# Kernel optimization log

Hardware: AMD Instinct MI355X
Metric: run time of the kernel (lower is better)

The kernel has to match this reference:

```python
import jax, jax.numpy as jnp
import numpy as np

B, N_TOK, DIM, HEADS, FRAMES = 16, 1569, 768, 12, 8
HEAD_DIM = DIM // HEADS
N_SPACE = (N_TOK - 1) // FRAMES  # 196
EPS = 1e-6


def _ln(x, w, b):
    m = jnp.mean(x, axis=-1, keepdims=True)
    v = jnp.var(x, axis=-1, keepdims=True)
    return (x - m) * jax.lax.rsqrt(v + EPS) * w + b


def _sdpa(q, k, v):
    # q: [..., Sq, d], k/v: [..., Sk, d]
    s = jnp.einsum('...qd,...kd->...qk', q, k) * (HEAD_DIM ** -0.5)
    return jnp.einsum('...qk,...kd->...qd', jax.nn.softmax(s, axis=-1), v)


def _divided_attn(x, w_qkv, b_qkv, w_proj, b_proj, mode):
    # Faithful translation of DividedAttention.forward
    Bb, N, D = x.shape
    h, d, f = HEADS, HEAD_DIM, FRAMES
    n = (N - 1) // f
    qkv = x @ w_qkv + b_qkv                      # [B, N, 3D]
    q, k, v = jnp.split(qkv, 3, axis=-1)
    q, k, v = (t.reshape(Bb, N, h, d).transpose(0, 2, 1, 3) for t in (q, k, v))  # [B,h,N,d]
    # global cls-token attention over ALL tokens
    cls_out = _sdpa(q[:, :, :1], k, v)           # [B,h,1,d]
    # local tokens: split (f n) per einops pattern 'b (f n) d'
    q_, k_, v_ = (t[:, :, 1:].reshape(Bb, h, f, n, d) for t in (q, k, v))
    if mode == 'time':
        # '(b n) f d': batch over spatial positions, attend over frames
        q_, k_, v_ = (t.transpose(0, 1, 3, 2, 4) for t in (q_, k_, v_))  # [B,h,n,f,d]
        r = n
    else:
        # '(b f) n d': batch over frames, attend over spatial positions
        r = f
    cls_k = jnp.broadcast_to(k[:, :, None, :1], (Bb, h, r, 1, d))
    cls_v = jnp.broadcast_to(v[:, :, None, :1], (Bb, h, r, 1, d))
    out = _sdpa(q_,
                jnp.concatenate([cls_k, k_], axis=3),
                jnp.concatenate([cls_v, v_], axis=3))   # [B,h,r,seq,d]
    if mode == 'time':
        out = out.transpose(0, 1, 3, 2, 4)       # back to [B,h,f,n,d]
    out = out.reshape(Bb, h, N - 1, d)
    out = jnp.concatenate([cls_out, out], axis=2)          # [B,h,N,d]
    out = out.transpose(0, 2, 1, 3).reshape(Bb, N, D)      # 'b n (h d)'
    return out @ w_proj + b_proj


def setup_inputs() -> dict:
    key = jax.random.key(0)
    ks = jax.random.split(key, 8)
    s = 0.02
    return {
        'x': jax.random.normal(ks[0], (B, N_TOK, DIM), jnp.float32),
        'norm1_w': jnp.ones((DIM,), jnp.float32),
        'norm1_b': jnp.zeros((DIM,), jnp.float32),
        'norm2_w': jnp.ones((DIM,), jnp.float32),
        'norm2_b': jnp.zeros((DIM,), jnp.float32),
        'norm3_w': jnp.ones((DIM,), jnp.float32),
        'norm3_b': jnp.zeros((DIM,), jnp.float32),
        'time_qkv_w': jax.random.normal(ks[1], (DIM, 3 * DIM), jnp.float32) * s,
        'time_qkv_b': jnp.zeros((3 * DIM,), jnp.float32),
        'time_proj_w': jax.random.normal(ks[2], (DIM, DIM), jnp.float32) * s,
        'time_proj_b': jnp.zeros((DIM,), jnp.float32),
        'space_qkv_w': jax.random.normal(ks[3], (DIM, 3 * DIM), jnp.float32) * s,
        'space_qkv_b': jnp.zeros((3 * DIM,), jnp.float32),
        'space_proj_w': jax.random.normal(ks[4], (DIM, DIM), jnp.float32) * s,
        'space_proj_b': jnp.zeros((DIM,), jnp.float32),
        'mlp_w1': jax.random.normal(ks[5], (DIM, 4 * DIM), jnp.float32) * s,
        'mlp_b1': jnp.zeros((4 * DIM,), jnp.float32),
        'mlp_w2': jax.random.normal(ks[6], (4 * DIM, DIM), jnp.float32) * s,
        'mlp_b2': jnp.zeros((DIM,), jnp.float32),
    }


def reference(x, norm1_w, norm1_b, norm2_w, norm2_b, norm3_w, norm3_b,
              time_qkv_w, time_qkv_b, time_proj_w, time_proj_b,
              space_qkv_w, space_qkv_b, space_proj_w, space_proj_b,
              mlp_w1, mlp_b1, mlp_w2, mlp_b2):
    # DividedSpaceTimeBlock.forward
    t = _divided_attn(_ln(x, norm3_w, norm3_b),
                      time_qkv_w, time_qkv_b, time_proj_w, time_proj_b, 'time')
    x = x + t
    s = _divided_attn(_ln(x, norm1_w, norm1_b),
                      space_qkv_w, space_qkv_b, space_proj_w, space_proj_b, 'space')
    x = x + s
    h = jax.nn.gelu(_ln(x, norm2_w, norm2_b) @ mlp_w1 + mlp_b1)
    return x + h @ mlp_w2 + mlp_b2
```

## Files before the change

### kernel.cpp

```cpp
#include <hip/hip_runtime.h>
#include <cstdint>
#include <cstddef>

typedef unsigned short u16;
typedef __attribute__((ext_vector_type(8))) short short8;
typedef __attribute__((ext_vector_type(4))) float f32x4;

#define BB 16
#define NT 1569
#define DIM 768
#define NH 12
#define HD 64
#define FR 8
#define NS 196
#define MROWS (BB*NT)
#define NKEY 197

__device__ __forceinline__ float bf2f(u16 h) {
    return __uint_as_float(((unsigned int)h) << 16);
}
__device__ __forceinline__ u16 f2bf(float f) {
    unsigned int u = __float_as_uint(f);
    u += 0x7fff + ((u >> 16) & 1);
    return (u16)(u >> 16);
}
__device__ __forceinline__ void gload_lds16(const u16* g, u16* l) {
    __builtin_amdgcn_global_load_lds(
        (const __attribute__((address_space(1))) void*)g,
        (__attribute__((address_space(3))) void*)l, 16, 0, 0);
}

template<bool IBF>
__global__ __launch_bounds__(256) void ln_kernel(const void* __restrict__ xin,
        const float* __restrict__ w, const float* __restrict__ b,
        u16* __restrict__ out) {
    int row = blockIdx.x;
    size_t base = (size_t)row * DIM;
    int tid = threadIdx.x;
    float v0, v1, v2;
    if (IBF) {
        const u16* x = (const u16*)xin;
        v0 = bf2f(x[base + tid]); v1 = bf2f(x[base + tid + 256]); v2 = bf2f(x[base + tid + 512]);
    } else {
        const float* x = (const float*)xin;
        v0 = x[base + tid]; v1 = x[base + tid + 256]; v2 = x[base + tid + 512];
    }
    float s = v0 + v1 + v2;
    float q = v0*v0 + v1*v1 + v2*v2;
    #pragma unroll
    for (int o = 32; o >= 1; o >>= 1) {
        s += __shfl_xor(s, o, 64);
        q += __shfl_xor(q, o, 64);
    }
    __shared__ float rs[4], rq[4];
    int wave = tid >> 6, lane = tid & 63;
    if (lane == 0) { rs[wave] = s; rq[wave] = q; }
    __syncthreads();
    float S = rs[0]+rs[1]+rs[2]+rs[3];
    float Q = rq[0]+rq[1]+rq[2]+rq[3];
    float mean = S * (1.0f/DIM);
    float var  = Q * (1.0f/DIM) - mean*mean;
    float inv  = rsqrtf(var + 1e-6f);
    out[base+tid]     = f2bf((v0-mean)*inv*w[tid]     + b[tid]);
    out[base+tid+256] = f2bf((v1-mean)*inv*w[tid+256] + b[tid+256]);
    out[base+tid+512] = f2bf((v2-mean)*inv*w[tid+512] + b[tid+512]);
}

__global__ __launch_bounds__(256) void wconv_kernel(const float* __restrict__ in,
        u16* __restrict__ out, int K, int N) {
    __shared__ float tile[32][33];
    int n0 = blockIdx.x * 32, k0 = blockIdx.y * 32;
    int tx = threadIdx.x & 31, ty = threadIdx.x >> 5;
    #pragma unroll
    for (int i = 0; i < 32; i += 8)
        tile[ty+i][tx] = in[(size_t)(k0+ty+i)*N + n0+tx];
    __syncthreads();
    #pragma unroll
    for (int i = 0; i < 32; i += 8)
        out[(size_t)(n0+ty+i)*K + k0+tx] = f2bf(tile[tx][ty+i]);
}

template<int EPI, bool OBF, bool RBF>
__global__ __launch_bounds__(256) void gemm_kernel(
        const u16* __restrict__ A, const u16* __restrict__ BT,
        const float* __restrict__ bias, const void* __restrict__ resid,
        void* __restrict__ Cout, int M, int N, int K, int num_m, int num_n) {
    __shared__ u16 lsA[128*32];
    __shared__ u16 lsB[128*32];
    const int GRP = 16;
    int pid = blockIdx.x;
    int gsz = GRP * num_n;
    int gid = pid / gsz;
    int rem = pid - gid*gsz;
    int m0b = gid * GRP;
    int msz = num_m - m0b; if (msz > GRP) msz = GRP;
    int pm = m0b + rem % msz;
    int pn = rem / msz;
    int row0 = pm * 128, col0 = pn * 128;
    int tid = threadIdx.x;
    int wave = tid >> 6, lane = tid & 63;
    int wm = (wave >> 1) * 64, wn = (wave & 1) * 64;
    int lrow = lane & 15, quad = lane >> 4;
    int srow = lane >> 2, scol = (lane & 3) * 8;
    const u16* gAp[2]; const u16* gBp[2];
    u16* lA[2]; u16* lB[2];
    #pragma unroll
    for (int i = 0; i < 2; ++i) {
        int r = wave*32 + i*16 + srow;
        int gr = row0 + r; if (gr > M-1) gr = M-1;
        gAp[i] = A  + (size_t)gr*K + scol;
        gBp[i] = BT + (size_t)(col0 + r)*K + scol;
        lA[i] = &lsA[(wave*32 + i*16)*32];
        lB[i] = &lsB[(wave*32 + i*16)*32];
    }
    f32x4 acc[4][4] = {};
    for (int k0 = 0; k0 < K; k0 += 32) {
        #pragma unroll
        for (int i = 0; i < 2; ++i) {
            gload_lds16(gAp[i] + k0, lA[i]);
            gload_lds16(gBp[i] + k0, lB[i]);
        }
        __syncthreads();
        short8 af[4], bfr[4];
        #pragma unroll
        for (int t = 0; t < 4; ++t)
            af[t] = *(const short8*)&lsA[(wm + t*16 + lrow)*32 + quad*8];
        #pragma unroll
        for (int t = 0; t < 4; ++t)
            bfr[t] = *(const short8*)&lsB[(wn + t*16 + lrow)*32 + quad*8];
        #pragma unroll
        for (int i = 0; i < 4; ++i)
            #pragma unroll
            for (int j = 0; j < 4; ++j)
                acc[i][j] = __builtin_amdgcn_mfma_f32_16x16x32_bf16(af[i], bfr[j], acc[i][j], 0, 0, 0);
        __syncthreads();
    }
    #pragma unroll
    for (int i = 0; i < 4; ++i) {
      #pragma unroll
      for (int j = 0; j < 4; ++j) {
        int gn = col0 + wn + j*16 + lrow;
        float bv = bias[gn];
        #pragma unroll
        for (int r = 0; r < 4; ++r) {
            int gm = row0 + wm + i*16 + quad*4 + r;
            if (gm < M) {
                float v = acc[i][j][r] + bv;
                if (EPI == 1) {
                    size_t ridx = (size_t)gm*N + gn;
                    v += RBF ? bf2f(((const u16*)resid)[ridx]) : ((const float*)resid)[ridx];
                }
                if (EPI == 2) {
                    float z = 0.7978845608028654f*(v + 0.044715f*v*v*v);
                    float t = 1.0f - 2.0f/(__expf(2.0f*z) + 1.0f);
                    v = 0.5f*v*(1.0f + t);
                }
                if (OBF) ((u16*)Cout)[(size_t)gm*N + gn] = f2bf(v);
                else     ((float*)Cout)[(size_t)gm*N + gn] = v;
            }
        }
      }
    }
}

__global__ __launch_bounds__(256) void attn_cls_kernel(const u16* __restrict__ qkv,
        u16* __restrict__ out) {
    __shared__ float s[NT];
    __shared__ float qf[64];
    __shared__ float part[4][64];
    __shared__ float red[4];
    int b = blockIdx.x / NH, h = blockIdx.x % NH;
    size_t base = ((size_t)b*NT)*(3*DIM) + h*HD;
    int tid = threadIdx.x;
    if (tid < 64) qf[tid] = bf2f(qkv[base + tid]);
    __syncthreads();
    float lmax = -1e30f;
    for (int t = tid; t < NT; t += 256) {
        const u16* kp = qkv + base + (size_t)t*(3*DIM) + DIM;
        float a0=0,a1=0,a2=0,a3=0;
        #pragma unroll
        for (int d = 0; d < 64; d += 4) {
            a0 += qf[d]  *bf2f(kp[d]);
            a1 += qf[d+1]*bf2f(kp[d+1]);
            a2 += qf[d+2]*bf2f(kp[d+2]);
            a3 += qf[d+3]*bf2f(kp[d+3]);
        }
        float sc = (a0+a1+a2+a3)*0.125f;
        s[t] = sc;
        lmax = fmaxf(lmax, sc);
    }
    #pragma unroll
    for (int o = 32; o >= 1; o >>= 1) lmax = fmaxf(lmax, __shfl_xor(lmax, o, 64));
    if ((tid&63) == 0) red[tid>>6] = lmax;
    __syncthreads();
    float m = fmaxf(fmaxf(red[0],red[1]), fmaxf(red[2],red[3]));
    float lsum = 0.f;
    for (int t = tid; t < NT; t += 256) { float e = __expf(s[t]-m); s[t] = e; lsum += e; }
    #pragma unroll
    for (int o = 32; o >= 1; o >>= 1) lsum += __shfl_xor(lsum, o, 64);
    __syncthreads();
    if ((tid&63) == 0) red[tid>>6] = lsum;
    __syncthreads();
    float inv = 1.0f/(red[0]+red[1]+red[2]+red[3]);
    int d = tid & 63, g = tid >> 6;
    float a = 0.f;
    for (int t = g; t < NT; t += 4)
        a += s[t]*bf2f(qkv[base + (size_t)t*(3*DIM) + 2*DIM + d]);
    part[g][d] = a;
    __syncthreads();
    if (tid < 64) {
        float o = (part[0][tid]+part[1][tid]+part[2][tid]+part[3][tid])*inv;
        out[((size_t)b*NT)*DIM + h*HD + tid] = f2bf(o);
    }
}

__global__ __launch_bounds__(256) void attn_time_kernel(const u16* __restrict__ qkv,
        u16* __restrict__ out) {
    __shared__ float qs[8][68], ks[9][68], vs[9][68];
    __shared__ float pr[8][12];
    int bid = blockIdx.x;
    int n = bid % NS; int rem = bid / NS; int h = rem % NH; int b = rem / NH;
    size_t base = ((size_t)b*NT)*(3*DIM) + h*HD;
    int tid = threadIdx.x;
    for (int idx = tid; idx < 512; idx += 256) {
        int f = idx >> 6, d = idx & 63;
        int tok = 1 + f*NS + n;
        size_t p = base + (size_t)tok*(3*DIM) + d;
        qs[f][d]   = bf2f(qkv[p]);
        ks[f+1][d] = bf2f(qkv[p + DIM]);
        vs[f+1][d] = bf2f(qkv[p + 2*DIM]);
    }
    if (tid < 64) {
        ks[0][tid] = bf2f(qkv[base + DIM + tid]);
        vs[0][tid] = bf2f(qkv[base + 2*DIM + tid]);
    }
    __syncthreads();
    if (tid < 72) {
        int fq = tid / 9, kk = tid % 9;
        float a0=0,a1=0,a2=0,a3=0;
        #pragma unroll
        for (int d = 0; d < 64; d += 4) {
            a0 += qs[fq][d]  *ks[kk][d];
            a1 += qs[fq][d+1]*ks[kk][d+1];
            a2 += qs[fq][d+2]*ks[kk][d+2];
            a3 += qs[fq][d+3]*ks[kk][d+3];
        }
        pr[fq][kk] = (a0+a1+a2+a3)*0.125f;
    }
    __syncthreads();
    if (tid < 8) {
        float m = -1e30f;
        #pragma unroll
        for (int kk = 0; kk < 9; ++kk) m = fmaxf(m, pr[tid][kk]);
        float sum = 0.f;
        #pragma unroll
        for (int kk = 0; kk < 9; ++kk) { float e = __expf(pr[tid][kk]-m); pr[tid][kk] = e; sum += e; }
        float inv = 1.0f/sum;
        #pragma unroll
        for (int kk = 0; kk < 9; ++kk) pr[tid][kk] *= inv;
    }
    __syncthreads();
    for (int idx = tid; idx < 512; idx += 256) {
        int fq = idx >> 6, d = idx & 63;
        float a = 0.f;
        #pragma unroll
        for (int kk = 0; kk < 9; ++kk) a += pr[fq][kk]*vs[kk][d];
        int tok = 1 + fq*NS + n;
        out[((size_t)b*NT + tok)*DIM + h*HD + d] = f2bf(a);
    }
}

#define VSTR 232
__global__ __launch_bounds__(256, 2) void attn_space_kernel(const u16* __restrict__ qkv,
        u16* __restrict__ out) {
    __shared__ u16 VT[64*VSTR];
    __shared__ u16 Ps[4][16*VSTR];
    int bid = blockIdx.x;
    int b = bid / (NH*FR); int rem = bid % (NH*FR); int h = rem / FR; int f = rem % FR;
    size_t base = ((size_t)b*NT)*(3*DIM) + (size_t)h*HD;
    int tid = threadIdx.x;
    int wave = tid >> 6, lane = tid & 63;
    int cb = lane & 15, quad = lane >> 4;

    for (int idx = tid; idx < NKEY*64; idx += 256) {
        int d = idx / NKEY, key = idx - d*NKEY;
        int tok = (key == 0) ? 0 : (1 + f*NS + key - 1);
        VT[d*VSTR + key] = qkv[base + (size_t)tok*(3*DIM) + 2*DIM + d];
    }
    for (int idx = tid; idx < 64*(VSTR-NKEY); idx += 256) {
        int d = idx / (VSTR-NKEY), c = idx - d*(VSTR-NKEY);
        VT[d*VSTR + NKEY + c] = 0;
    }
    for (int idx = tid; idx < 4*16*(VSTR-208); idx += 256) {
        int r = idx / (VSTR-208), c = idx - r*(VSTR-208);
        ((u16*)Ps)[r*VSTR + 208 + c] = 0;
    }
    __syncthreads();

    for (int qt = wave; qt < 13; qt += 4) {
        int q0 = qt*16;
        int qrow = q0 + cb; if (qrow > 195) qrow = 195;
        const u16* qp = qkv + base + (size_t)(1 + f*NS + qrow)*(3*DIM);
        short8 a0 = *(const short8*)(qp + quad*8);
        short8 a1 = *(const short8*)(qp + 32 + quad*8);
        f32x4 sacc[13];
        #pragma unroll
        for (int kt = 0; kt < 13; ++kt) {
            int key = kt*16 + cb; if (key > 196) key = 196;
            int ktok = (key == 0) ? 0 : (1 + f*NS + key - 1);
            const u16* kp = qkv + base + (size_t)ktok*(3*DIM) + DIM;
            short8 b0 = *(const short8*)(kp + quad*8);
            short8 b1 = *(const short8*)(kp + 32 + quad*8);
            f32x4 z = {0.f, 0.f, 0.f, 0.f};
            z = __builtin_amdgcn_mfma_f32_16x16x32_bf16(a0, b0, z, 0, 0, 0);
            z = __builtin_amdgcn_mfma_f32_16x16x32_bf16(a1, b1, z, 0, 0, 0);
            sacc[kt] = z;
        }
        bool last_ok = (cb < 5);
        float mx[4] = {-1e30f, -1e30f, -1e30f, -1e30f};
        #pragma unroll
        for (int kt = 0; kt < 13; ++kt) {
            bool ok = (kt < 12) || last_ok;
            #pragma unroll
            for (int r = 0; r < 4; ++r) {
                float v = sacc[kt][r] * 0.125f;
                sacc[kt][r] = v;
                if (ok) mx[r] = fmaxf(mx[r], v);
            }
        }
        #pragma unroll
        for (int off = 1; off < 16; off <<= 1)
            #pragma unroll
            for (int r = 0; r < 4; ++r)
                mx[r] = fmaxf(mx[r], __shfl_xor(mx[r], off, 64));
        float sum[4] = {0.f, 0.f, 0.f, 0.f};
        u16* prow = &Ps[wave][0];
        #pragma unroll
        for (int kt = 0; kt < 13; ++kt) {
            bool ok = (kt < 12) || last_ok;
            #pragma unroll
            for (int r = 0; r < 4; ++r) {
                float e = ok ? __expf(sacc[kt][r] - mx[r]) : 0.f;
                sum[r] += e;
                prow[(quad*4 + r)*VSTR + kt*16 + cb] = f2bf(e);
            }
        }
        #pragma unroll
        for (int off = 1; off < 16; off <<= 1)
            #pragma unroll
            for (int r = 0; r < 4; ++r)
                sum[r] += __shfl_xor(sum[r], off, 64);
        short8 pf[7];
        #pragma unroll
        for (int ks = 0; ks < 7; ++ks)
            pf[ks] = *(const short8*)&Ps[wave][cb*VSTR + ks*32 + quad*8];
        f32x4 oacc[4];
        #pragma unroll
        for (int nt = 0; nt < 4; ++nt) {
            f32x4 z = {0.f, 0.f, 0.f, 0.f};
            #pragma unroll
            for (int ks = 0; ks < 7; ++ks) {
                short8 vf = *(const short8*)&VT[(nt*16 + cb)*VSTR + ks*32 + quad*8];
                z = __builtin_amdgcn_mfma_f32_16x16x32_bf16(pf[ks], vf, z, 0, 0, 0);
            }
            oacc[nt] = z;
        }
        float inv[4];
        #pragma unroll
        for (int r = 0; r < 4; ++r) inv[r] = 1.0f / sum[r];
        #pragma unroll
        for (int r = 0; r < 4; ++r) {
            int qr = q0 + quad*4 + r;
            if (qr < 196) {
                size_t orow = ((size_t)b*NT + 1 + (size_t)f*NS + qr)*DIM + (size_t)h*HD;
                #pragma unroll
                for (int nt = 0; nt < 4; ++nt)
                    out[orow + nt*16 + cb] = f2bf(oacc[nt][r] * inv[r]);
            }
        }
    }
}

extern "C" void kernel_launch(void* const* d_in, const int* in_sizes, int n_in,
                              void* d_out, int out_size, void* d_ws, size_t ws_size,
                              hipStream_t stream) {
    const float* x          = (const float*)d_in[0];
    const float* norm1_w    = (const float*)d_in[1];
    const float* norm1_b    = (const float*)d_in[2];
    const float* norm2_w    = (const float*)d_in[3];
    const float* norm2_b    = (const float*)d_in[4];
    const float* norm3_w    = (const float*)d_in[5];
    const float* norm3_b    = (const float*)d_in[6];
    const float* t_qkv_w    = (const float*)d_in[7];
    const float* t_qkv_b    = (const float*)d_in[8];
    const float* t_proj_w   = (const float*)d_in[9];
    const float* t_proj_b   = (const float*)d_in[10];
    const float* s_qkv_w    = (const float*)d_in[11];
    const float* s_qkv_b    = (const float*)d_in[12];
    const float* s_proj_w   = (const float*)d_in[13];
    const float* s_proj_b   = (const float*)d_in[14];
    const float* mlp_w1     = (const float*)d_in[15];
    const float* mlp_b1     = (const float*)d_in[16];
    const float* mlp_w2     = (const float*)d_in[17];
    const float* mlp_b2     = (const float*)d_in[18];
    float* out = (float*)d_out;

    char* ws = (char*)d_ws;
    const size_t M = MROWS;
    u16*  qkv  = (u16*)(ws);
    u16*  attn = (u16*)(ws + M*2304*2);
    u16*  hbuf = (u16*)(ws);
    u16*  xn   = (u16*)(ws + M*3072*2);
    u16*  x1   = (u16*)(ws + M*3072*2 + M*768*2);
    char* wsp  = ws + M*3072*2 + M*768*2 + M*768*4;
    u16* wqT_t = (u16*)(wsp);                 wsp += 2304*768*2;
    u16* wqT_s = (u16*)(wsp);                 wsp += 2304*768*2;
    u16* wpT_t = (u16*)(wsp);                 wsp += 768*768*2;
    u16* wpT_s = (u16*)(wsp);                 wsp += 768*768*2;
    u16* w1T   = (u16*)(wsp);                 wsp += 3072*768*2;
    u16* w2T   = (u16*)(wsp);

    wconv_kernel<<<dim3(2304/32, 768/32), 256, 0, stream>>>(t_qkv_w, wqT_t, 768, 2304);
    wconv_kernel<<<dim3(2304/32, 768/32), 256, 0, stream>>>(s_qkv_w, wqT_s, 768, 2304);
    wconv_kernel<<<dim3(768/32, 768/32), 256, 0, stream>>>(t_proj_w, wpT_t, 768, 768);
    wconv_kernel<<<dim3(768/32, 768/32), 256, 0, stream>>>(s_proj_w, wpT_s, 768, 768);
    wconv_kernel<<<dim3(3072/32, 768/32), 256, 0, stream>>>(mlp_w1, w1T, 768, 3072);
    wconv_kernel<<<dim3(768/32, 3072/32), 256, 0, stream>>>(mlp_w2, w2T, 3072, 768);

    const int GM = (MROWS + 127) / 128;

    ln_kernel<false><<<MROWS, 256, 0, stream>>>(x, norm3_w, norm3_b, xn);
    gemm_kernel<0, true, false><<<GM*(2304/128), 256, 0, stream>>>(xn, wqT_t, t_qkv_b, nullptr, qkv, MROWS, 2304, 768, GM, 2304/128);
    attn_cls_kernel <<<BB*NH, 256, 0, stream>>>(qkv, attn);
    attn_time_kernel<<<BB*NH*NS, 256, 0, stream>>>(qkv, attn);
    gemm_kernel<1, true, false><<<GM*(768/128), 256, 0, stream>>>(attn, wpT_t, t_proj_b, x, x1, MROWS, 768, 768, GM, 768/128);

    ln_kernel<true><<<MROWS, 256, 0, stream>>>(x1, norm1_w, norm1_b, xn);
    gemm_kernel<0, true, false><<<GM*(2304/128), 256, 0, stream>>>(xn, wqT_s, s_qkv_b, nullptr, qkv, MROWS, 2304, 768, GM, 2304/128);
    attn_cls_kernel  <<<BB*NH, 256, 0, stream>>>(qkv, attn);
    attn_space_kernel<<<BB*NH*FR, 256, 0, stream>>>(qkv, attn);
    gemm_kernel<1, false, true><<<GM*(768/128), 256, 0, stream>>>(attn, wpT_s, s_proj_b, x1, out, MROWS, 768, 768, GM, 768/128);

    ln_kernel<false><<<MROWS, 256, 0, stream>>>(out, norm2_w, norm2_b, xn);
    gemm_kernel<2, true, false><<<GM*(3072/128), 256, 0, stream>>>(xn, w1T, mlp_b1, nullptr, hbuf, MROWS, 3072, 768, GM, 3072/128);
    gemm_kernel<1, false, false><<<GM*(768/128), 256, 0, stream>>>(hbuf, w2T, mlp_b2, out, out, MROWS, 768, 3072, GM, 768/128);
}
```

Before: 1.560 ms.

## Template GEMM tile width and K depth, split CLS attention across key chunks

The GEMM kernel is templated on N-tile width and K-step depth. The QKV and MLP1 GEMMs use 128x256 tiles and every GEMM uses BK=64, for more reuse per LDS load and fewer barriers per K loop. The CLS-token attention, which used only B*H blocks, is split into 8 key chunks that produce partial max, sum and output, followed by a small merge kernel, to expose more parallelism. The cost is higher register and LDS use per GEMM block, which may lower occupancy, plus one extra launch per attention stage.

```diff
diff --git a/kernel.cpp b/kernel.cpp
--- a/kernel.cpp
+++ b/kernel.cpp
@@ -80,13 +80,16 @@
         out[(size_t)(n0+ty+i)*K + k0+tx] = f2bf(tile[tx][ty+i]);
 }
 
-template<int EPI, bool OBF, bool RBF>
+template<int TN, int BK, int EPI, bool OBF, bool RBF>
 __global__ __launch_bounds__(256) void gemm_kernel(
         const u16* __restrict__ A, const u16* __restrict__ BT,
         const float* __restrict__ bias, const void* __restrict__ resid,
         void* __restrict__ Cout, int M, int N, int K, int num_m, int num_n) {
-    __shared__ u16 lsA[128*32];
-    __shared__ u16 lsB[128*32];
+    constexpr int BN = 32 * TN;
+    constexpr int AI = BK / 16;
+    constexpr int BI = BN * BK / 2048;
+    __shared__ u16 lsA[128*BK];
+    __shared__ u16 lsB[BN*BK];
     const int GRP = 16;
     int pid = blockIdx.x;
     int gsz = GRP * num_n;
@@ -96,50 +99,57 @@
     int msz = num_m - m0b; if (msz > GRP) msz = GRP;
     int pm = m0b + rem % msz;
     int pn = rem / msz;
-    int row0 = pm * 128, col0 = pn * 128;
+    int row0 = pm * 128, col0 = pn * BN;
     int tid = threadIdx.x;
     int wave = tid >> 6, lane = tid & 63;
-    int wm = (wave >> 1) * 64, wn = (wave & 1) * 64;
-    int lrow = lane & 15, quad = lane >> 4;
-    int srow = lane >> 2, scol = (lane & 3) * 8;
-    const u16* gAp[2]; const u16* gBp[2];
-    u16* lA[2]; u16* lB[2];
-    #pragma unroll
-    for (int i = 0; i < 2; ++i) {
-        int r = wave*32 + i*16 + srow;
+    int wm = (wave >> 1) * 64, wn = (wave & 1) * 16 * TN;
+    int cb = lane & 15, quad = lane >> 4;
+    const u16* gAp[AI]; const u16* gBp[BI];
+    u16* lA[AI]; u16* lB[BI];
+    #pragma unroll
+    for (int i = 0; i < AI; ++i) {
+        int e = (wave*AI + i)*512 + lane*8;
+        int r = e / BK, c = e % BK;
         int gr = row0 + r; if (gr > M-1) gr = M-1;
-        gAp[i] = A  + (size_t)gr*K + scol;
-        gBp[i] = BT + (size_t)(col0 + r)*K + scol;
-        lA[i] = &lsA[(wave*32 + i*16)*32];
-        lB[i] = &lsB[(wave*32 + i*16)*32];
-    }
-    f32x4 acc[4][4] = {};
-    for (int k0 = 0; k0 < K; k0 += 32) {
-        #pragma unroll
-        for (int i = 0; i < 2; ++i) {
-            gload_lds16(gAp[i] + k0, lA[i]);
-            gload_lds16(gBp[i] + k0, lB[i]);
-        }
+        gAp[i] = A + (size_t)gr*K + c;
+        lA[i] = &lsA[(wave*AI + i)*512];
+    }
+    #pragma unroll
+    for (int i = 0; i < BI; ++i) {
+        int e = (wave*BI + i)*512 + lane*8;
+        int r = e / BK, c = e % BK;
+        gBp[i] = BT + (size_t)(col0 + r)*K + c;
+        lB[i] = &lsB[(wave*BI + i)*512];
+    }
+    f32x4 acc[4][TN] = {};
+    for (int k0 = 0; k0 < K; k0 += BK) {
+        #pragma unroll
+        for (int i = 0; i < AI; ++i) gload_lds16(gAp[i] + k0, lA[i]);
+        #pragma unroll
+        for (int i = 0; i < BI; ++i) gload_lds16(gBp[i] + k0, lB[i]);
         __syncthreads();
-        short8 af[4], bfr[4];
-        #pragma unroll
-        for (int t = 0; t < 4; ++t)
-            af[t] = *(const short8*)&lsA[(wm + t*16 + lrow)*32 + quad*8];
-        #pragma unroll
-        for (int t = 0; t < 4; ++t)
-            bfr[t] = *(const short8*)&lsB[(wn + t*16 + lrow)*32 + quad*8];
-        #pragma unroll
-        for (int i = 0; i < 4; ++i)
-            #pragma unroll
-            for (int j = 0; j < 4; ++j)
-                acc[i][j] = __builtin_amdgcn_mfma_f32_16x16x32_bf16(af[i], bfr[j], acc[i][j], 0, 0, 0);
+        #pragma unroll
+        for (int ks = 0; ks < BK/32; ++ks) {
+            short8 af[4], bfr[TN];
+            #pragma unroll
+            for (int t = 0; t < 4; ++t)
+                af[t] = *(const short8*)&lsA[(wm + t*16 + cb)*BK + ks*32 + quad*8];
+            #pragma unroll
+            for (int j = 0; j < TN; ++j)
+                bfr[j] = *(const short8*)&lsB[(wn + j*16 + cb)*BK + ks*32 + quad*8];
+            #pragma unroll
+            for (int i = 0; i < 4; ++i)
+                #pragma unroll
+                for (int j = 0; j < TN; ++j)
+                    acc[i][j] = __builtin_amdgcn_mfma_f32_16x16x32_bf16(af[i], bfr[j], acc[i][j], 0, 0, 0);
+        }
         __syncthreads();
     }
     #pragma unroll
     for (int i = 0; i < 4; ++i) {
       #pragma unroll
-      for (int j = 0; j < 4; ++j) {
-        int gn = col0 + wn + j*16 + lrow;
+      for (int j = 0; j < TN; ++j) {
+        int gn = col0 + wn + j*16 + cb;
         float bv = bias[gn];
         #pragma unroll
         for (int r = 0; r < 4; ++r) {
@@ -163,20 +173,23 @@
     }
 }
 
-__global__ __launch_bounds__(256) void attn_cls_kernel(const u16* __restrict__ qkv,
-        u16* __restrict__ out) {
-    __shared__ float s[NT];
+__global__ __launch_bounds__(256) void attn_cls_part(const u16* __restrict__ qkv,
+        float* __restrict__ part) {
     __shared__ float qf[64];
-    __shared__ float part[4][64];
+    __shared__ float p[256];
     __shared__ float red[4];
-    int b = blockIdx.x / NH, h = blockIdx.x % NH;
-    size_t base = ((size_t)b*NT)*(3*DIM) + h*HD;
+    __shared__ float pacc[4][64];
+    int bid = blockIdx.x;
+    int c = bid & 7; int h = (bid >> 3) % NH; int b = bid / (8*NH);
+    size_t base = ((size_t)b*NT)*(3*DIM) + (size_t)h*HD;
+    int k0 = c * 197;
+    int nk = NT - k0; if (nk > 197) nk = 197;
     int tid = threadIdx.x;
     if (tid < 64) qf[tid] = bf2f(qkv[base + tid]);
     __syncthreads();
-    float lmax = -1e30f;
-    for (int t = tid; t < NT; t += 256) {
-        const u16* kp = qkv + base + (size_t)t*(3*DIM) + DIM;
+    float sc = -1e30f;
+    if (tid < nk) {
+        const u16* kp = qkv + base + (size_t)(k0 + tid)*(3*DIM) + DIM;
         float a0=0,a1=0,a2=0,a3=0;
         #pragma unroll
         for (int d = 0; d < 64; d += 4) {
@@ -185,33 +198,52 @@
             a2 += qf[d+2]*bf2f(kp[d+2]);
             a3 += qf[d+3]*bf2f(kp[d+3]);
         }
-        float sc = (a0+a1+a2+a3)*0.125f;
-        s[t] = sc;
-        lmax = fmaxf(lmax, sc);
-    }
+        sc = (a0+a1+a2+a3)*0.125f;
+    }
+    float lmax = sc;
     #pragma unroll
     for (int o = 32; o >= 1; o >>= 1) lmax = fmaxf(lmax, __shfl_xor(lmax, o, 64));
     if ((tid&63) == 0) red[tid>>6] = lmax;
     __syncthreads();
     float m = fmaxf(fmaxf(red[0],red[1]), fmaxf(red[2],red[3]));
-    float lsum = 0.f;
-    for (int t = tid; t < NT; t += 256) { float e = __expf(s[t]-m); s[t] = e; lsum += e; }
+    float e = (tid < nk) ? __expf(sc - m) : 0.f;
+    p[tid] = e;
+    float lsum = e;
     #pragma unroll
     for (int o = 32; o >= 1; o >>= 1) lsum += __shfl_xor(lsum, o, 64);
     __syncthreads();
     if ((tid&63) == 0) red[tid>>6] = lsum;
     __syncthreads();
-    float inv = 1.0f/(red[0]+red[1]+red[2]+red[3]);
+    float s = red[0]+red[1]+red[2]+red[3];
     int d = tid & 63, g = tid >> 6;
     float a = 0.f;
-    for (int t = g; t < NT; t += 4)
-        a += s[t]*bf2f(qkv[base + (size_t)t*(3*DIM) + 2*DIM + d]);
-    part[g][d] = a;
-    __syncthreads();
-    if (tid < 64) {
-        float o = (part[0][tid]+part[1][tid]+part[2][tid]+part[3][tid])*inv;
-        out[((size_t)b*NT)*DIM + h*HD + tid] = f2bf(o);
-    }
+    for (int kk = g; kk < nk; kk += 4)
+        a += p[kk]*bf2f(qkv[base + (size_t)(k0+kk)*(3*DIM) + 2*DIM + d]);
+    pacc[g][d] = a;
+    __syncthreads();
+    float* pc = part + (size_t)bid*66;
+    if (tid == 0) { pc[0] = m; pc[1] = s; }
+    if (tid < 64)
+        pc[2+tid] = pacc[0][tid]+pacc[1][tid]+pacc[2][tid]+pacc[3][tid];
+}
+
+__global__ __launch_bounds__(64) void attn_cls_merge(const float* __restrict__ part,
+        u16* __restrict__ out) {
+    int bid = blockIdx.x;
+    int b = bid / NH, h = bid % NH;
+    int tid = threadIdx.x;
+    const float* pc = part + (size_t)bid*8*66;
+    float mstar = -1e30f;
+    #pragma unroll
+    for (int c = 0; c < 8; ++c) mstar = fmaxf(mstar, pc[c*66]);
+    float S = 0.f, O = 0.f;
+    #pragma unroll
+    for (int c = 0; c < 8; ++c) {
+        float al = __expf(pc[c*66] - mstar);
+        S += pc[c*66 + 1] * al;
+        O += pc[c*66 + 2 + tid] * al;
+    }
+    out[((size_t)b*NT)*DIM + h*HD + tid] = f2bf(O / S);
 }
 
 __global__ __launch_bounds__(256) void attn_time_kernel(const u16* __restrict__ qkv,
@@ -412,6 +444,7 @@
     u16*  hbuf = (u16*)(ws);
     u16*  xn   = (u16*)(ws + M*3072*2);
     u16*  x1   = (u16*)(ws + M*3072*2 + M*768*2);
+    float* clsp = (float*)(ws + M*3072*2 + M*768*2 + M*768*2);
     char* wsp  = ws + M*3072*2 + M*768*2 + M*768*4;
     u16* wqT_t = (u16*)(wsp);                 wsp += 2304*768*2;
     u16* wqT_s = (u16*)(wsp);                 wsp += 2304*768*2;
@@ -430,18 +463,20 @@
     const int GM = (MROWS + 127) / 128;
 
     ln_kernel<false><<<MROWS, 256, 0, stream>>>(x, norm3_w, norm3_b, xn);
-    gemm_kernel<0, true, false><<<GM*(2304/128), 256, 0, stream>>>(xn, wqT_t, t_qkv_b, nullptr, qkv, MROWS, 2304, 768, GM, 2304/128);
-    attn_cls_kernel <<<BB*NH, 256, 0, stream>>>(qkv, attn);
+    gemm_kernel<8, 64, 0, true, false><<<GM*(2304/256), 256, 0, stream>>>(xn, wqT_t, t_qkv_b, nullptr, qkv, MROWS, 2304, 768, GM, 2304/256);
+    attn_cls_part <<<BB*NH*8, 256, 0, stream>>>(qkv, clsp);
+    attn_cls_merge<<<BB*NH, 64, 0, stream>>>(clsp, attn);
     attn_time_kernel<<<BB*NH*NS, 256, 0, stream>>>(qkv, attn);
-    gemm_kernel<1, true, false><<<GM*(768/128), 256, 0, stream>>>(attn, wpT_t, t_proj_b, x, x1, MROWS, 768, 768, GM, 768/128);
+    gemm_kernel<4, 64, 1, true, false><<<GM*(768/128), 256, 0, stream>>>(attn, wpT_t, t_proj_b, x, x1, MROWS, 768, 768, GM, 768/128);
 
     ln_kernel<true><<<MROWS, 256, 0, stream>>>(x1, norm1_w, norm1_b, xn);
-    gemm_kernel<0, true, false><<<GM*(2304/128), 256, 0, stream>>>(xn, wqT_s, s_qkv_b, nullptr, qkv, MROWS, 2304, 768, GM, 2304/128);
-    attn_cls_kernel  <<<BB*NH, 256, 0, stream>>>(qkv, attn);
+    gemm_kernel<8, 64, 0, true, false><<<GM*(2304/256), 256, 0, stream>>>(xn, wqT_s, s_qkv_b, nullptr, qkv, MROWS, 2304, 768, GM, 2304/256);
+    attn_cls_part <<<BB*NH*8, 256, 0, stream>>>(qkv, clsp);
+    attn_cls_merge<<<BB*NH, 64, 0, stream>>>(clsp, attn);
     attn_space_kernel<<<BB*NH*FR, 256, 0, stream>>>(qkv, attn);
-    gemm_kernel<1, false, true><<<GM*(768/128), 256, 0, stream>>>(attn, wpT_s, s_proj_b, x1, out, MROWS, 768, 768, GM, 768/128);
+    gemm_kernel<4, 64, 1, false, true><<<GM*(768/128), 256, 0, stream>>>(attn, wpT_s, s_proj_b, x1, out, MROWS, 768, 768, GM, 768/128);
 
     ln_kernel<false><<<MROWS, 256, 0, stream>>>(out, norm2_w, norm2_b, xn);
-    gemm_kernel<2, true, false><<<GM*(3072/128), 256, 0, stream>>>(xn, w1T, mlp_b1, nullptr, hbuf, MROWS, 3072, 768, GM, 3072/128);
-    gemm_kernel<1, false, false><<<GM*(768/128), 256, 0, stream>>>(hbuf, w2T, mlp_b2, out, out, MROWS, 768, 3072, GM, 768/128);
-}
+    gemm_kernel<8, 64, 2, true, false><<<GM*(3072/256), 256, 0, stream>>>(xn, w1T, mlp_b1, nullptr, hbuf, MROWS, 3072, 768, GM, 3072/256);
+    gemm_kernel<4, 64, 1, false, false><<<GM*(768/128), 256, 0, stream>>>(hbuf, w2T, mlp_b2, out, out, MROWS, 768, 3072, GM, 768/128);
+}
```

Measured after the change: 1.925 ms. 23.4% more time.
